# Performance work log

Hardware: AMD Instinct MI355X
Metric: run time of the kernel (lower is better)

Reference implementation:

```python
import jax, jax.numpy as jnp
import numpy as np

N_NODES = 50000
N_EDGES = 800000
IN_C, HID_C, OUT_C = 256, 512, 256


def _linear_params(key, fan_in, fan_out):
    kw, kb = jax.random.split(key)
    bound = 1.0 / np.sqrt(fan_in)
    w = jax.random.uniform(kw, (fan_in, fan_out), jnp.float32, -bound, bound)
    b = jax.random.uniform(kb, (fan_out,), jnp.float32, -bound, bound)
    return w, b


def setup_inputs() -> dict:
    key = jax.random.key(0)
    ks = jax.random.split(key, 6)
    x = jax.random.normal(ks[0], (N_NODES, IN_C), jnp.float32)
    src = jax.random.randint(ks[1], (N_EDGES,), 0, N_NODES, jnp.int32)
    dst = jax.random.randint(ks[2], (N_EDGES,), 0, N_NODES, jnp.int32)
    w1, b1 = _linear_params(ks[3], IN_C, HID_C)
    w2, b2 = _linear_params(ks[4], HID_C, HID_C)
    w3, b3 = _linear_params(ks[5], HID_C, OUT_C)
    eps = jnp.zeros((), jnp.float32)  # GIN learnable eps, init 0
    return {"x": x, "src": src, "dst": dst,
            "w1": w1, "b1": b1, "eps1": eps,
            "w2": w2, "b2": b2, "eps2": eps,
            "w3": w3, "b3": b3, "eps3": eps}


def _gin_conv(h, src, dst, w, b, eps, n_nodes):
    # aggregate: (A @ h)[i] = sum over edges (src->dst==i) of h[src]
    agg = jax.ops.segment_sum(h[src], dst, num_segments=n_nodes)
    return ((1.0 + eps) * h + agg) @ w + b


def reference(x, src, dst, w1, b1, eps1, w2, b2, eps2, w3, b3, eps3):
    n = x.shape[0]
    # eval-mode forward: dropout is identity
    h = jax.nn.relu(_gin_conv(x, src, dst, w1, b1, eps1, n))
    h = jax.nn.relu(_gin_conv(h, src, dst, w2, b2, eps2, n))
    return _gin_conv(h, src, dst, w3, b3, eps3, n)
```

## Files before the change

kernel.cpp:

```cpp
#include <hip/hip_runtime.h>

#define N_NODES 50000
#define N_EDGES 800000
#define IN_C 256
#define HID_C 512
#define OUT_C 256
#define M_PAD 50048
#define NPASS 8
#define PASS_SHIFT 13

typedef unsigned short u16;
typedef unsigned int   u32;
typedef u16  u16x4 __attribute__((ext_vector_type(4)));
typedef u16  u16x8 __attribute__((ext_vector_type(8)));
typedef short s16x8 __attribute__((ext_vector_type(8)));
typedef float f32x4 __attribute__((ext_vector_type(4)));

__device__ __forceinline__ float bf2f(u16 h) {
    u32 u = ((u32)h) << 16;
    return __builtin_bit_cast(float, u);
}
__device__ __forceinline__ u16 f2bf(float f) {
    u32 u = __builtin_bit_cast(u32, f);
    u32 r = u + 0x7fffu + ((u >> 16) & 1u);
    return (u16)(r >> 16);
}
__device__ __forceinline__ void gload16(const void* g, void* l) {
    __builtin_amdgcn_global_load_lds(
        (const __attribute__((address_space(1))) u32*)g,
        (__attribute__((address_space(3))) u32*)l, 16, 0, 0);
}
__device__ __forceinline__ int swz4(int r) { return (r ^ (r >> 2)) & 3; }

__global__ void k_hist8(const int* __restrict__ src, const int* __restrict__ dst,
                        int* __restrict__ cnt8) {
    int e = blockIdx.x * 256 + threadIdx.x;
    if (e < N_EDGES) {
        int q = src[e] >> PASS_SHIFT;
        atomicAdd(&cnt8[dst[e] * NPASS + q], 1);
    }
}

__global__ void k_partial(const int* __restrict__ cnt, int* __restrict__ bsum, int total) {
    __shared__ int s[256];
    int i = blockIdx.x * 256 + threadIdx.x;
    int v = (i < total) ? cnt[i] : 0;
    s[threadIdx.x] = v; __syncthreads();
    for (int o = 128; o > 0; o >>= 1) {
        if (threadIdx.x < o) s[threadIdx.x] += s[threadIdx.x + o];
        __syncthreads();
    }
    if (threadIdx.x == 0) bsum[blockIdx.x] = s[0];
}

__global__ void k_scanb(int* __restrict__ bsum, int nb) {
    __shared__ int s[256];
    int carry = 0;
    for (int base = 0; base < nb; base += 256) {
        int i = base + threadIdx.x;
        int v = (i < nb) ? bsum[i] : 0;
        s[threadIdx.x] = v; __syncthreads();
        for (int o = 1; o < 256; o <<= 1) {
            int t = (threadIdx.x >= o) ? s[threadIdx.x - o] : 0;
            __syncthreads();
            s[threadIdx.x] += t;
            __syncthreads();
        }
        int tot = s[255];
        if (i < nb) bsum[i] = s[threadIdx.x] - v + carry;
        carry += tot;
        __syncthreads();
    }
}

__global__ void k_rowptr8(const int* __restrict__ cnt, const int* __restrict__ bsum,
                          int* __restrict__ rp, int* __restrict__ cur, int total) {
    __shared__ int s[256];
    int i = blockIdx.x * 256 + threadIdx.x;
    int v = (i < total) ? cnt[i] : 0;
    s[threadIdx.x] = v; __syncthreads();
    for (int o = 1; o < 256; o <<= 1) {
        int t = (threadIdx.x >= o) ? s[threadIdx.x - o] : 0;
        __syncthreads();
        s[threadIdx.x] += t;
        __syncthreads();
    }
    int excl = s[threadIdx.x] - v + bsum[blockIdx.x];
    if (i < total) { rp[i] = excl; cur[i] = excl; }
    if (i == total - 1) rp[total] = excl + v;
}

__global__ void k_scatter8(const int* __restrict__ src, const int* __restrict__ dst,
                           int* __restrict__ cur, int* __restrict__ col) {
    int e = blockIdx.x * 256 + threadIdx.x;
    if (e < N_EDGES) {
        int sv = src[e];
        int q = sv >> PASS_SHIFT;
        int p = atomicAdd(&cur[dst[e] * NPASS + q], 1);
        col[p] = sv;
    }
}

__global__ void k_wt(const float* __restrict__ w, u16* __restrict__ wt, int K, int N) {
    int idx = blockIdx.x * 256 + threadIdx.x;
    if (idx >= K * N) return;
    int n = idx / K, k = idx - n * K;
    wt[idx] = f2bf(w[(size_t)k * N + n]);
}

__global__ void k_x2bf(const float* __restrict__ x, u16* __restrict__ xb) {
    int i = blockIdx.x * 256 + threadIdx.x;
    if (i < N_NODES * IN_C / 4) {
        float4 v = ((const float4*)x)[i];
        u16x4 o;
        o[0] = f2bf(v.x); o[1] = f2bf(v.y); o[2] = f2bf(v.z); o[3] = f2bf(v.w);
        ((u16x4*)xb)[i] = o;
    }
}

template <int C, int EPI>
__global__ __launch_bounds__(256) void k_agg_stream(
    const u16* __restrict__ sm, const int* __restrict__ rp8,
    const int* __restrict__ col, const float* __restrict__ eps,
    const float* __restrict__ bias, void* __restrict__ out) {
    constexpr int NSLAB = C / 64;
    const int slab  = blockIdx.x & (NSLAB - 1);
    const int chunk = blockIdx.x / NSLAB;
    const int gid = threadIdx.x >> 4;
    const int ln  = threadIdx.x & 15;
    const int ch0 = slab * 64 + ln * 4;
    const int n = chunk * 16 + gid;
    if (n >= N_NODES) return;
    const float ep = 1.f + eps[0];

    const int rs = rp8[n * NPASS];
    const int re = rp8[n * NPASS + NPASS];
    float a0 = 0.f, a1 = 0.f, a2 = 0.f, a3 = 0.f;
    int e = rs;
    for (; e + 4 <= re; e += 4) {
        int s0 = col[e], s1 = col[e + 1], s2 = col[e + 2], s3 = col[e + 3];
        u16x4 v0 = *(const u16x4*)(sm + (size_t)s0 * C + ch0);
        u16x4 v1 = *(const u16x4*)(sm + (size_t)s1 * C + ch0);
        u16x4 v2 = *(const u16x4*)(sm + (size_t)s2 * C + ch0);
        u16x4 v3 = *(const u16x4*)(sm + (size_t)s3 * C + ch0);
        a0 += bf2f(v0[0]) + bf2f(v1[0]) + bf2f(v2[0]) + bf2f(v3[0]);
        a1 += bf2f(v0[1]) + bf2f(v1[1]) + bf2f(v2[1]) + bf2f(v3[1]);
        a2 += bf2f(v0[2]) + bf2f(v1[2]) + bf2f(v2[2]) + bf2f(v3[2]);
        a3 += bf2f(v0[3]) + bf2f(v1[3]) + bf2f(v2[3]) + bf2f(v3[3]);
    }
    for (; e < re; e++) {
        int s0 = col[e];
        u16x4 v0 = *(const u16x4*)(sm + (size_t)s0 * C + ch0);
        a0 += bf2f(v0[0]); a1 += bf2f(v0[1]); a2 += bf2f(v0[2]); a3 += bf2f(v0[3]);
    }

    u16x4 sv = *(const u16x4*)(sm + (size_t)n * C + ch0);
    float r0 = fmaf(ep, bf2f(sv[0]), a0);
    float r1 = fmaf(ep, bf2f(sv[1]), a1);
    float r2 = fmaf(ep, bf2f(sv[2]), a2);
    float r3 = fmaf(ep, bf2f(sv[3]), a3);
    if constexpr (EPI == 0) {
        u16x4 o;
        o[0] = f2bf(r0); o[1] = f2bf(r1); o[2] = f2bf(r2); o[3] = f2bf(r3);
        *(u16x4*)((u16*)out + (size_t)n * C + ch0) = o;
    } else {
        float4 bv = *(const float4*)(bias + ch0);
        float4 o;
        o.x = r0 + bv.x; o.y = r1 + bv.y; o.z = r2 + bv.z; o.w = r3 + bv.w;
        *(float4*)((float*)out + (size_t)n * C + ch0) = o;
    }
}

template <int K, int EPI>
__global__ __launch_bounds__(256, 2) void gemm_k(
    const u16* __restrict__ A, const u16* __restrict__ Wt,
    const float* __restrict__ bias, void* __restrict__ out,
    int N, int grid_n) {
    __shared__ u16 Als[128 * 32];
    __shared__ u16 Bls[128 * 32];
    const int tid  = threadIdx.x;
    const int wave = tid >> 6, lane = tid & 63;
    const int wm = wave >> 1, wn = wave & 1;
    const int bm = blockIdx.x / grid_n, bn = blockIdx.x % grid_n;
    const int m0 = bm * 128, n0 = bn * 128;
    const int sr = lane >> 2, sc = lane & 3;
    const int fr = lane & 15, kg = lane >> 4;

    f32x4 acc[4][4];
#pragma unroll
    for (int i = 0; i < 4; i++)
#pragma unroll
        for (int j = 0; j < 4; j++) acc[i][j] = (f32x4){0.f, 0.f, 0.f, 0.f};

    for (int kk = 0; kk < K; kk += 32) {
#pragma unroll
        for (int i = 0; i < 2; i++) {
            int rl = wave * 32 + i * 16 + sr;
            int c  = sc ^ swz4(rl);
            gload16(A  + (size_t)(m0 + rl) * K + kk + c * 8,
                    &Als[(wave * 32 + i * 16) * 32]);
            gload16(Wt + (size_t)(n0 + rl) * K + kk + c * 8,
                    &Bls[(wave * 32 + i * 16) * 32]);
        }
        asm volatile("s_waitcnt vmcnt(0)" ::: "memory");
        __syncthreads();

        s16x8 af[4], bfr[4];
#pragma unroll
        for (int mi = 0; mi < 4; mi++) {
            int r = wm * 64 + mi * 16 + fr;
            int c = kg ^ swz4(r);
            af[mi] = *(const s16x8*)&Als[r * 32 + c * 8];
        }
#pragma unroll
        for (int ni = 0; ni < 4; ni++) {
            int r = wn * 64 + ni * 16 + fr;
            int c = kg ^ swz4(r);
            bfr[ni] = *(const s16x8*)&Bls[r * 32 + c * 8];
        }
#pragma unroll
        for (int mi = 0; mi < 4; mi++)
#pragma unroll
            for (int ni = 0; ni < 4; ni++)
                acc[mi][ni] = __builtin_amdgcn_mfma_f32_16x16x32_bf16(
                    af[mi], bfr[ni], acc[mi][ni], 0, 0, 0);
        __syncthreads();
    }

#pragma unroll
    for (int ni = 0; ni < 4; ni++) {
        int cn = n0 + wn * 64 + ni * 16 + fr;
        float bv = 0.f;
        if constexpr (EPI == 0) bv = bias[cn];
#pragma unroll
        for (int mi = 0; mi < 4; mi++) {
            int rb = m0 + wm * 64 + mi * 16 + kg * 4;
#pragma unroll
            for (int j = 0; j < 4; j++) {
                int r = rb + j;
                if (r < N_NODES) {
                    float v = acc[mi][ni][j];
                    if constexpr (EPI == 0) {
                        v += bv;
                        v = v > 0.f ? v : 0.f;
                    }
                    ((u16*)out)[(size_t)r * N + cn] = f2bf(v);
                }
            }
        }
    }
}

extern "C" void kernel_launch(void* const* d_in, const int* in_sizes, int n_in,
                              void* d_out, int out_size, void* d_ws, size_t ws_size,
                              hipStream_t stream) {
    const float* x    = (const float*)d_in[0];
    const int*   src  = (const int*)d_in[1];
    const int*   dst  = (const int*)d_in[2];
    const float* w1   = (const float*)d_in[3];
    const float* b1   = (const float*)d_in[4];
    const float* eps1 = (const float*)d_in[5];
    const float* w2   = (const float*)d_in[6];
    const float* b2   = (const float*)d_in[7];
    const float* eps2 = (const float*)d_in[8];
    const float* w3   = (const float*)d_in[9];
    const float* b3   = (const float*)d_in[10];
    const float* eps3 = (const float*)d_in[11];

    char* ws = (char*)d_ws;
    size_t off = 0;
    auto take = [&](size_t bytes) {
        char* p = ws + off;
        off += (bytes + 255) & ~(size_t)255;
        return p;
    };
    const int TOT8 = N_NODES * NPASS;
    int* cnt8 = (int*)take((size_t)TOT8 * 4);
    int* rp8  = (int*)take((size_t)(TOT8 + 1) * 4);
    int* cur8 = (int*)take((size_t)TOT8 * 4);
    int* bsum = (int*)take(2048 * 4);
    int* col  = (int*)take((size_t)N_EDGES * 4);
    u16* w1t  = (u16*)take((size_t)IN_C * HID_C * 2);
    u16* w2t  = (u16*)take((size_t)HID_C * HID_C * 2);
    u16* w3t  = (u16*)take((size_t)HID_C * OUT_C * 2);
    u16* A0   = (u16*)take((size_t)M_PAD * IN_C * 2);
    u16* h1   = (u16*)take((size_t)M_PAD * HID_C * 2);
    u16* A1   = (u16*)take((size_t)M_PAD * HID_C * 2);
    u16* xb = A1;
    u16* h2 = h1;
    u16* g3 = A1;

    const int NB8 = (TOT8 + 255) / 256;
    const int NE  = (N_EDGES + 255) / 256;

    hipMemsetAsync(cnt8, 0, (size_t)TOT8 * 4, stream);
    k_hist8  <<<NE, 256, 0, stream>>>(src, dst, cnt8);
    k_partial<<<NB8, 256, 0, stream>>>(cnt8, bsum, TOT8);
    k_scanb  <<<1, 256, 0, stream>>>(bsum, NB8);
    k_rowptr8<<<NB8, 256, 0, stream>>>(cnt8, bsum, rp8, cur8, TOT8);
    k_scatter8<<<NE, 256, 0, stream>>>(src, dst, cur8, col);

    k_wt<<<(IN_C * HID_C + 255) / 256, 256, 0, stream>>>(w1, w1t, IN_C, HID_C);
    k_wt<<<(HID_C * HID_C + 255) / 256, 256, 0, stream>>>(w2, w2t, HID_C, HID_C);
    k_wt<<<(HID_C * OUT_C + 255) / 256, 256, 0, stream>>>(w3, w3t, HID_C, OUT_C);
    k_x2bf<<<(N_NODES * IN_C / 4 + 255) / 256, 256, 0, stream>>>(x, xb);

    const int NCH  = (N_NODES + 15) / 16;
    const int G512 = NCH * 8;
    const int G256 = NCH * 4;

    k_agg_stream<IN_C, 0><<<G256, 256, 0, stream>>>(xb, rp8, col, eps1, nullptr, A0);
    gemm_k<IN_C, 0><<<391 * (HID_C / 128), 256, 0, stream>>>(
        A0, w1t, b1, h1, HID_C, HID_C / 128);

    k_agg_stream<HID_C, 0><<<G512, 256, 0, stream>>>(h1, rp8, col, eps2, nullptr, A1);
    gemm_k<HID_C, 0><<<391 * (HID_C / 128), 256, 0, stream>>>(
        A1, w2t, b2, h2, HID_C, HID_C / 128);

    gemm_k<HID_C, 1><<<391 * (OUT_C / 128), 256, 0, stream>>>(
        h2, w3t, nullptr, g3, OUT_C, OUT_C / 128);
    k_agg_stream<OUT_C, 1><<<G256, 256, 0, stream>>>(g3, rp8, col, eps3, b3, (float*)d_out);
}
```

Baseline: 478.6 us.

## Double GEMM K-tile to 64 and stage epilogue through LDS for coalesced stores

The bf16 MFMA GEMM now loads a 64-wide K slice per iteration with an 8-way XOR swizzle, so it hits half as many barriers and issues more MFMAs per load phase. The epilogue writes bias+ReLU results into a padded LDS tile (row stride 130) and then stores full rows with 16-byte vector writes, replacing the scattered 2-byte global stores. This uses more LDS per block, which could reduce occupancy. The 16-byte LDS reads on the 260-byte row stride are not 16-byte aligned.

```diff
diff --git a/kernel.cpp b/kernel.cpp
--- a/kernel.cpp
+++ b/kernel.cpp
@@ -30,7 +30,6 @@
         (const __attribute__((address_space(1))) u32*)g,
         (__attribute__((address_space(3))) u32*)l, 16, 0, 0);
 }
-__device__ __forceinline__ int swz4(int r) { return (r ^ (r >> 2)) & 3; }
 
 __global__ void k_hist8(const int* __restrict__ src, const int* __restrict__ dst,
                         int* __restrict__ cnt8) {
@@ -176,14 +175,15 @@
     const u16* __restrict__ A, const u16* __restrict__ Wt,
     const float* __restrict__ bias, void* __restrict__ out,
     int N, int grid_n) {
-    __shared__ u16 Als[128 * 32];
-    __shared__ u16 Bls[128 * 32];
+    __shared__ u16 smem[16640];
+    u16* Als = smem;
+    u16* Bls = smem + 8192;
     const int tid  = threadIdx.x;
     const int wave = tid >> 6, lane = tid & 63;
     const int wm = wave >> 1, wn = wave & 1;
     const int bm = blockIdx.x / grid_n, bn = blockIdx.x % grid_n;
     const int m0 = bm * 128, n0 = bn * 128;
-    const int sr = lane >> 2, sc = lane & 3;
+    const int sr = lane >> 3, sc = lane & 7;
     const int fr = lane & 15, kg = lane >> 4;
 
     f32x4 acc[4][4];
@@ -192,61 +192,74 @@
 #pragma unroll
         for (int j = 0; j < 4; j++) acc[i][j] = (f32x4){0.f, 0.f, 0.f, 0.f};
 
-    for (int kk = 0; kk < K; kk += 32) {
-#pragma unroll
-        for (int i = 0; i < 2; i++) {
-            int rl = wave * 32 + i * 16 + sr;
-            int c  = sc ^ swz4(rl);
-            gload16(A  + (size_t)(m0 + rl) * K + kk + c * 8,
-                    &Als[(wave * 32 + i * 16) * 32]);
-            gload16(Wt + (size_t)(n0 + rl) * K + kk + c * 8,
-                    &Bls[(wave * 32 + i * 16) * 32]);
+    for (int kk = 0; kk < K; kk += 64) {
+#pragma unroll
+        for (int i = 0; i < 4; i++) {
+            int rl = wave * 32 + i * 8 + sr;
+            int cs = sc ^ (rl & 7);
+            gload16(A  + (size_t)(m0 + rl) * K + kk + cs * 8,
+                    &Als[(wave * 32 + i * 8) * 64]);
+            gload16(Wt + (size_t)(n0 + rl) * K + kk + cs * 8,
+                    &Bls[(wave * 32 + i * 8) * 64]);
         }
         asm volatile("s_waitcnt vmcnt(0)" ::: "memory");
         __syncthreads();
 
-        s16x8 af[4], bfr[4];
+#pragma unroll
+        for (int k2 = 0; k2 < 2; k2++) {
+            s16x8 af[4], bfr[4];
+#pragma unroll
+            for (int mi = 0; mi < 4; mi++) {
+                int r = wm * 64 + mi * 16 + fr;
+                int c = (k2 * 4 + kg) ^ (r & 7);
+                af[mi] = *(const s16x8*)&Als[r * 64 + c * 8];
+            }
+#pragma unroll
+            for (int ni = 0; ni < 4; ni++) {
+                int r = wn * 64 + ni * 16 + fr;
+                int c = (k2 * 4 + kg) ^ (r & 7);
+                bfr[ni] = *(const s16x8*)&Bls[r * 64 + c * 8];
+            }
+#pragma unroll
+            for (int mi = 0; mi < 4; mi++)
+#pragma unroll
+                for (int ni = 0; ni < 4; ni++)
+                    acc[mi][ni] = __builtin_amdgcn_mfma_f32_16x16x32_bf16(
+                        af[mi], bfr[ni], acc[mi][ni], 0, 0, 0);
+        }
+        __syncthreads();
+    }
+
+    u16* Cls = smem;
+#pragma unroll
+    for (int ni = 0; ni < 4; ni++) {
+        int c = wn * 64 + ni * 16 + fr;
+        float bv = 0.f;
+        if constexpr (EPI == 0) bv = bias[n0 + c];
 #pragma unroll
         for (int mi = 0; mi < 4; mi++) {
-            int r = wm * 64 + mi * 16 + fr;
-            int c = kg ^ swz4(r);
-            af[mi] = *(const s16x8*)&Als[r * 32 + c * 8];
-        }
-#pragma unroll
-        for (int ni = 0; ni < 4; ni++) {
-            int r = wn * 64 + ni * 16 + fr;
-            int c = kg ^ swz4(r);
-            bfr[ni] = *(const s16x8*)&Bls[r * 32 + c * 8];
-        }
-#pragma unroll
-        for (int mi = 0; mi < 4; mi++)
-#pragma unroll
-            for (int ni = 0; ni < 4; ni++)
-                acc[mi][ni] = __builtin_amdgcn_mfma_f32_16x16x32_bf16(
-                    af[mi], bfr[ni], acc[mi][ni], 0, 0, 0);
-        __syncthreads();
-    }
-
-#pragma unroll
-    for (int ni = 0; ni < 4; ni++) {
-        int cn = n0 + wn * 64 + ni * 16 + fr;
-        float bv = 0.f;
-        if constexpr (EPI == 0) bv = bias[cn];
-#pragma unroll
-        for (int mi = 0; mi < 4; mi++) {
-            int rb = m0 + wm * 64 + mi * 16 + kg * 4;
 #pragma unroll
             for (int j = 0; j < 4; j++) {
-                int r = rb + j;
-                if (r < N_NODES) {
-                    float v = acc[mi][ni][j];
-                    if constexpr (EPI == 0) {
-                        v += bv;
-                        v = v > 0.f ? v : 0.f;
-                    }
-                    ((u16*)out)[(size_t)r * N + cn] = f2bf(v);
+                int r = wm * 64 + mi * 16 + kg * 4 + j;
+                float v = acc[mi][ni][j];
+                if constexpr (EPI == 0) {
+                    v += bv;
+                    v = v > 0.f ? v : 0.f;
                 }
+                Cls[r * 130 + c] = f2bf(v);
             }
+        }
+    }
+    __syncthreads();
+
+    const int r2 = tid >> 1;
+    const int cb = (tid & 1) * 64;
+    if (m0 + r2 < N_NODES) {
+        u16* orow = (u16*)out + (size_t)(m0 + r2) * N + n0 + cb;
+#pragma unroll
+        for (int k = 0; k < 8; k++) {
+            u16x8 val = *(const u16x8*)&Cls[r2 * 130 + cb + k * 8];
+            *(u16x8*)(orow + k * 8) = val;
         }
     }
 }
```

Result: faster. 459.1 us (-4.1%).
